# Kernel optimization log

Measured on AMD Instinct MI355X. Metric: run time of the kernel, lower is better.

The kernel has to match this reference:

```python
import jax, jax.numpy as jnp
import numpy as np

V, H, L = 32000, 2048, 4
B, S = 4, 1024


def setup_inputs() -> dict:
    key = jax.random.key(0)
    ks = jax.random.split(key, 10)
    input_ids = jax.random.randint(ks[0], (B, S), 0, V)
    emb = jax.random.normal(ks[1], (V, H), dtype=jnp.float32)
    # ternary quantized weights in {-1, 0, +1}, stored as int8
    layer_wq = jax.random.randint(ks[2], (L, H, H), -1, 2).astype(jnp.int8)
    layer_scale = jax.random.normal(ks[3], (L, H, 1), dtype=jnp.float32)
    layer_bias = jax.random.normal(ks[4], (L, H), dtype=jnp.float32)
    out_wq = jax.random.randint(ks[5], (V, H), -1, 2).astype(jnp.int8)
    out_scale = jax.random.normal(ks[6], (V, 1), dtype=jnp.float32)
    out_bias = jax.random.normal(ks[7], (V,), dtype=jnp.float32)
    return {
        "input_ids": input_ids,
        "emb": emb,
        "layer_wq": layer_wq,
        "layer_scale": layer_scale,
        "layer_bias": layer_bias,
        "out_wq": out_wq,
        "out_scale": out_scale,
        "out_bias": out_bias,
    }


def _bit_linear(x, wq, scale, bias):
    # dequantize ternary int8 weight: [out,in] * [out,1] -> fp32, then x @ W^T + b
    w = wq.astype(jnp.float32) * scale
    return jnp.einsum("bsh,oh->bso", x, w) + bias


def reference(input_ids, emb, layer_wq, layer_scale, layer_bias, out_wq, out_scale, out_bias):
    x = emb[input_ids]  # [B,S,H]
    for i in range(L):
        x = jax.nn.relu(_bit_linear(x, layer_wq[i], layer_scale[i], layer_bias[i]))
    logits = _bit_linear(x, out_wq, out_scale, out_bias)  # [B,S,V]
    return logits
```

## Files before the change

kernel.cpp:

```cpp
#include <hip/hip_runtime.h>
#include <hip/hip_bf16.h>
#include <stdint.h>
#include <stddef.h>

#define GLOBAL_AS __attribute__((address_space(1)))
#define LDS_AS __attribute__((address_space(3)))

typedef __attribute__((ext_vector_type(4))) float f32x4;
typedef __attribute__((ext_vector_type(8))) short bf16x8;
typedef __attribute__((ext_vector_type(4))) int   i32x4;

template<int N> struct ICn { static constexpr int value = N; };

__device__ __forceinline__ unsigned short f2bf(float f) {
  unsigned u = __float_as_uint(f);
  u += 0x7FFFu + ((u >> 16) & 1u);
  return (unsigned short)(u >> 16);
}

__device__ __forceinline__ void load_lds16(const void* g, void* l) {
  __builtin_amdgcn_global_load_lds((const GLOBAL_AS void*)g, (LDS_AS void*)l, 16, 0, 0);
}

template<int IMM, typename T>
__device__ __forceinline__ void ds_read128t(T &d, unsigned addr) {
  asm volatile("ds_read_b128 %0, %1 offset:%c2"
               : "=&v"(d) : "v"(addr), "i"(IMM));
}

__global__ __launch_bounds__(256) void detect_dtype_k(const int* __restrict__ w,
                                                      int* __restrict__ flag) {
  __shared__ int bad;
  if (threadIdx.x == 0) bad = 0;
  __syncthreads();
  int b = 0;
  for (int i = threadIdx.x; i < 4096; i += 256) {
    int v = w[i];
    if (v < -1 || v > 1) b = 1;
  }
  if (b) bad = 1;
  __syncthreads();
  if (threadIdx.x == 0) *flag = bad ? 0 : 1;
}

__global__ __launch_bounds__(256) void gather_emb_k(const int* __restrict__ ids,
                                                    const float* __restrict__ emb,
                                                    unsigned short* __restrict__ x) {
  const int t = blockIdx.x;
  const int row = ids[t];
  const float4* src = (const float4*)(emb + (size_t)row * 2048);
  const int e = threadIdx.x;
  float4 a = src[e * 2], b = src[e * 2 + 1];
  uint4 o;
  o.x = f2bf(a.x) | ((unsigned)f2bf(a.y) << 16);
  o.y = f2bf(a.z) | ((unsigned)f2bf(a.w) << 16);
  o.z = f2bf(b.x) | ((unsigned)f2bf(b.y) << 16);
  o.w = f2bf(b.z) | ((unsigned)f2bf(b.w) << 16);
  *(uint4*)(x + (size_t)t * 2048 + e * 8) = o;
}

__global__ __launch_bounds__(256) void convert_w_k(const void* __restrict__ src,
                                                   unsigned short* __restrict__ dst,
                                                   const int* __restrict__ flag) {
  const long long idx = ((long long)blockIdx.x * 256 + threadIdx.x) * 8;
  int v[8];
  if (*flag) {
    const int* s = (const int*)src + idx;
    const int4 a = *(const int4*)s;
    const int4 b = *(const int4*)(s + 4);
    v[0] = a.x; v[1] = a.y; v[2] = a.z; v[3] = a.w;
    v[4] = b.x; v[5] = b.y; v[6] = b.z; v[7] = b.w;
  } else {
    const uint2 u = *(const uint2*)((const char*)src + idx);
    v[0] = (char)(u.x); v[1] = (char)(u.x >> 8); v[2] = (char)(u.x >> 16); v[3] = (char)(u.x >> 24);
    v[4] = (char)(u.y); v[5] = (char)(u.y >> 8); v[6] = (char)(u.y >> 16); v[7] = (char)(u.y >> 24);
  }
  unsigned short o[8];
  #pragma unroll
  for (int k = 0; k < 8; ++k)
    o[k] = (v[k] == 0) ? 0 : ((v[k] > 0) ? 0x3F80 : 0xBF80);
  uint4 w;
  w.x = o[0] | ((unsigned)o[1] << 16);
  w.y = o[2] | ((unsigned)o[3] << 16);
  w.z = o[4] | ((unsigned)o[5] << 16);
  w.w = o[6] | ((unsigned)o[7] << 16);
  *(uint4*)(dst + idx) = w;
}

__global__ __launch_bounds__(256) void pack_w8_k(const void* __restrict__ src,
                                                 signed char* __restrict__ dst,
                                                 const int* __restrict__ flag) {
  const long long idx = ((long long)blockIdx.x * 256 + threadIdx.x) * 8;
  if (*flag) {
    const int* s = (const int*)src + idx;
    const int4 a = *(const int4*)s;
    const int4 b = *(const int4*)(s + 4);
    uint2 o;
    o.x = ((unsigned)(unsigned char)(signed char)a.x)       |
          ((unsigned)(unsigned char)(signed char)a.y << 8)  |
          ((unsigned)(unsigned char)(signed char)a.z << 16) |
          ((unsigned)(unsigned char)(signed char)a.w << 24);
    o.y = ((unsigned)(unsigned char)(signed char)b.x)       |
          ((unsigned)(unsigned char)(signed char)b.y << 8)  |
          ((unsigned)(unsigned char)(signed char)b.z << 16) |
          ((unsigned)(unsigned char)(signed char)b.w << 24);
    *(uint2*)(dst + idx) = o;
  } else {
    *(uint2*)(dst + idx) = *(const uint2*)((const char*)src + idx);
  }
}

__global__ __launch_bounds__(256) void colsum_k(const signed char* __restrict__ w,
                                                float* __restrict__ cs) {
  const int lane = threadIdx.x & 63;
  const int c = blockIdx.x * 4 + (threadIdx.x >> 6);
  const int4* p = (const int4*)(w + (size_t)c * 2048 + lane * 32);
  const int4 a = p[0], b = p[1];
  int wds[8] = {a.x, a.y, a.z, a.w, b.x, b.y, b.z, b.w};
  int s = 0;
  #pragma unroll
  for (int k = 0; k < 8; ++k)
    #pragma unroll
    for (int bb = 0; bb < 4; ++bb)
      s += (signed char)(wds[k] >> (8 * bb));
  #pragma unroll
  for (int o = 32; o; o >>= 1) s += __shfl_xor(s, o);
  if (lane == 0) cs[c] = (float)s;
}

__global__ __launch_bounds__(256) void rowquant_k(const unsigned short* __restrict__ x,
                                                  signed char* __restrict__ xq,
                                                  float* __restrict__ srow) {
  __shared__ float wmax[4];
  const int r = blockIdx.x;
  const int e = threadIdx.x;
  const uint4 u = *(const uint4*)(x + (size_t)r * 2048 + e * 8);
  unsigned wds[4] = {u.x, u.y, u.z, u.w};
  float v[8];
  #pragma unroll
  for (int k = 0; k < 4; ++k) {
    v[2 * k]     = __uint_as_float(wds[k] << 16);
    v[2 * k + 1] = __uint_as_float(wds[k] & 0xFFFF0000u);
  }
  float m = 0.0f;
  #pragma unroll
  for (int k = 0; k < 8; ++k) m = fmaxf(m, v[k]);
  #pragma unroll
  for (int o = 32; o; o >>= 1) m = fmaxf(m, __shfl_xor(m, o));
  if ((threadIdx.x & 63) == 0) wmax[threadIdx.x >> 6] = m;
  __syncthreads();
  const float mx = fmaxf(fmaxf(wmax[0], wmax[1]), fmaxf(wmax[2], wmax[3]));
  const float inv = mx > 0.0f ? 255.0f / mx : 0.0f;
  unsigned b[8];
  #pragma unroll
  for (int k = 0; k < 8; ++k) {
    int q = __float2int_rn(v[k] * inv - 127.5f);
    q = q < -128 ? -128 : (q > 127 ? 127 : q);
    b[k] = (unsigned)(unsigned char)(signed char)q;
  }
  uint2 o;
  o.x = b[0] | (b[1] << 8) | (b[2] << 16) | (b[3] << 24);
  o.y = b[4] | (b[5] << 8) | (b[6] << 16) | (b[7] << 24);
  *(uint2*)(xq + (size_t)r * 2048 + e * 8) = o;
  if (threadIdx.x == 0) srow[r] = mx * (1.0f / 255.0f);
}

__global__ __launch_bounds__(256) void gemm_bt_k(
    const unsigned short* __restrict__ A,
    const unsigned short* __restrict__ Bw,
    const float* __restrict__ scale,
    const float* __restrict__ bias,
    unsigned short* __restrict__ Cout,
    int M, int N, int K)
{
  __shared__ unsigned short As[128 * 64];
  __shared__ unsigned short Bs[128 * 64];

  const int tid  = threadIdx.x;
  const int lane = tid & 63;
  const int wid  = tid >> 6;
  const int wm   = wid >> 1;
  const int wn   = wid & 1;

  const int mBase = blockIdx.y * 128;
  const int nBase = blockIdx.x * 128;

  const int srow = lane >> 3;
  const int skel = (lane & 7) * 8;

  f32x4 acc[4][4];
  #pragma unroll
  for (int i = 0; i < 4; ++i)
    #pragma unroll
    for (int j = 0; j < 4; ++j)
      acc[i][j] = (f32x4){0.f, 0.f, 0.f, 0.f};

  for (int k0 = 0; k0 < K; k0 += 64) {
    #pragma unroll
    for (int j = 0; j < 4; ++j) {
      const int c = wid * 4 + j;
      const int row = c * 8 + srow;
      load_lds16(A  + (size_t)(mBase + row) * K + (k0 + skel), As + c * 512);
      load_lds16(Bw + (size_t)(nBase + row) * K + (k0 + skel), Bs + c * 512);
    }
    __syncthreads();

    #pragma unroll
    for (int s = 0; s < 2; ++s) {
      const int kk = s * 32 + (lane >> 4) * 8;
      bf16x8 af[4], bfr[4];
      #pragma unroll
      for (int i = 0; i < 4; ++i)
        af[i] = *(const bf16x8*)(As + (wm * 64 + i * 16 + (lane & 15)) * 64 + kk);
      #pragma unroll
      for (int j = 0; j < 4; ++j)
        bfr[j] = *(const bf16x8*)(Bs + (wn * 64 + j * 16 + (lane & 15)) * 64 + kk);
      #pragma unroll
      for (int i = 0; i < 4; ++i)
        #pragma unroll
        for (int j = 0; j < 4; ++j)
          acc[i][j] = __builtin_amdgcn_mfma_f32_16x16x32_bf16(af[i], bfr[j], acc[i][j], 0, 0, 0);
    }
    __syncthreads();
  }

  const int lr = lane >> 4;
  const int lc = lane & 15;
  #pragma unroll
  for (int j = 0; j < 4; ++j) {
    const int col = nBase + wn * 64 + j * 16 + lc;
    const float sc = scale[col];
    const float bs = bias[col];
    #pragma unroll
    for (int i = 0; i < 4; ++i) {
      const int r0 = mBase + wm * 64 + i * 16 + lr * 4;
      #pragma unroll
      for (int r = 0; r < 4; ++r) {
        float vv = fmaxf(acc[i][j][r] * sc + bs, 0.0f);
        Cout[(size_t)(r0 + r) * N + col] = f2bf(vv);
      }
    }
  }
}


#define RD_B8() do { \
  ds_read128t<PAR*32768 +    0>(bfr[0][0], vB0); ds_read128t<PAR*32768 +    0>(bfr[0][1], vB1); \
  ds_read128t<PAR*32768 + 2048>(bfr[1][0], vB0); ds_read128t<PAR*32768 + 2048>(bfr[1][1], vB1); \
  ds_read128t<PAR*32768 + 4096>(bfr[2][0], vB0); ds_read128t<PAR*32768 + 4096>(bfr[2][1], vB1); \
  ds_read128t<PAR*32768 + 6144>(bfr[3][0], vB0); ds_read128t<PAR*32768 + 6144>(bfr[3][1], vB1); \
} while (0)

#define RD_A2(dst, R) do { \
  ds_read128t<PAR*32768 + (R)*2048       >(dst[0][0], vA0); ds_read128t<PAR*32768 + (R)*2048       >(dst[0][1], vA1); \
  ds_read128t<PAR*32768 + (R)*2048 + 2048>(dst[1][0], vA0); ds_read128t<PAR*32768 + (R)*2048 + 2048>(dst[1][1], vA1); \
} while (0)

#define STAGE_A(h) do { if (t >= 1 && t + 1 < nt) { \
  load_lds16(pA[h][0], As + (PAR ^ 1) * 32768 + (h) * 16384 +        wid * 1024); \
  load_lds16(pA[h][1], As + (PAR ^ 1) * 32768 + (h) * 16384 + 8192 + wid * 1024); \
  pA[h][0] += 128; pA[h][1] += 128; } } while (0)

#define STAGE_B(h) do { if (t + 2 < nt) { \
  load_lds16(pB[h][0], Bs + PAR * 32768 + (h) * 16384 +        wid * 1024); \
  load_lds16(pB[h][1], Bs + PAR * 32768 + (h) * 16384 + 8192 + wid * 1024); \
  pB[h][0] += 128; pB[h][1] += 128; } } while (0)

#define SBAR0 __builtin_amdgcn_sched_barrier(0)

#define LGKM_WAIT(LG) \
  SBAR0; \
  asm volatile("s_waitcnt lgkmcnt(" #LG ")" ::: "memory"); \
  SBAR0;

#define MFMA_PH(IP, AF) \
  __builtin_amdgcn_s_setprio(1); \
  { _Pragma("unroll") for (int ii = 0; ii < 2; ++ii) { \
      _Pragma("unroll") for (int j = 0; j < 4; ++j) { \
        acc[(IP)*2+ii][j] = __builtin_amdgcn_mfma_i32_16x16x64_i8(AF[ii][0], bfr[j][0], acc[(IP)*2+ii][j], 0, 0, 0); \
        acc[(IP)*2+ii][j] = __builtin_amdgcn_mfma_i32_16x16x64_i8(AF[ii][1], bfr[j][1], acc[(IP)*2+ii][j], 0, 0, 0); \
  } } } \
  __builtin_amdgcn_s_setprio(0); \
  SBAR0;

__global__ __launch_bounds__(512) void gemm256i8_k(
    const signed char* __restrict__ Aq,
    const signed char* __restrict__ Bq,
    const float* __restrict__ scale,
    const float* __restrict__ bias,
    const float* __restrict__ srow,
    const float* __restrict__ colsum,
    float* __restrict__ C,
    int M, int N, int K)
{
  __shared__ signed char As[2 * 32768];
  __shared__ signed char Bs[2 * 32768];

  const int tid  = threadIdx.x;
  const int lane = tid & 63;
  const int wid  = tid >> 6;
  const int wm   = wid >> 2;
  const int wn   = wid & 3;
  const int l15  = lane & 15;
  const int l4   = lane >> 4;

  const int q    = gridDim.x >> 3;
  const int wgid = (blockIdx.x & 7) * q + (blockIdx.x >> 3);
  const int mBase = (wgid & 15) << 8;
  const int nBase = (wgid >> 4) << 8;

  const int gsw = ((lane & 7) ^ (lane >> 3)) * 16;

  const unsigned asB = (unsigned)(size_t)(const LDS_AS signed char*)As;
  const unsigned bsB = (unsigned)(size_t)(const LDS_AS signed char*)Bs;
  const unsigned x7  = (unsigned)(l15 & 7);
  const unsigned vA0 = asB + (wm << 14) + l15 * 128 + ((((unsigned)l4    ) ^ x7) << 4);
  const unsigned vA1 = asB + (wm << 14) + l15 * 128 + ((((unsigned)l4 + 4) ^ x7) << 4);
  const unsigned vB0 = bsB + (wn << 13) + l15 * 128 + ((((unsigned)l4    ) ^ x7) << 4);
  const unsigned vB1 = bsB + (wn << 13) + l15 * 128 + ((((unsigned)l4 + 4) ^ x7) << 4);

  const signed char* pA[2][2];
  const signed char* pB[2][2];
  #pragma unroll
  for (int h = 0; h < 2; ++h)
    #pragma unroll
    for (int j = 0; j < 2; ++j) {
      const int row = h * 128 + j * 64 + wid * 8 + (lane >> 3);
      pA[h][j] = Aq + (size_t)(mBase + row) * K + gsw;
      pB[h][j] = Bq + (size_t)(nBase + row) * K + gsw;
    }

  i32x4 acc[8][4];
  #pragma unroll
  for (int i = 0; i < 8; ++i)
    #pragma unroll
    for (int j = 0; j < 4; ++j)
      acc[i][j] = (i32x4){0, 0, 0, 0};

  const int nt = K >> 7;

  #pragma unroll
  for (int h = 0; h < 2; ++h)
    #pragma unroll
    for (int j = 0; j < 2; ++j)
      load_lds16(pA[h][j], As + h * 16384 + j * 8192 + wid * 1024);
  #pragma unroll
  for (int h = 0; h < 2; ++h)
    #pragma unroll
    for (int j = 0; j < 2; ++j)
      load_lds16(pB[h][j], Bs + h * 16384 + j * 8192 + wid * 1024);
  #pragma unroll
  for (int h = 0; h < 2; ++h)
    #pragma unroll
    for (int j = 0; j < 2; ++j)
      load_lds16(pA[h][j] + 128, As + 32768 + h * 16384 + j * 8192 + wid * 1024);
  #pragma unroll
  for (int h = 0; h < 2; ++h)
    #pragma unroll
    for (int j = 0; j < 2; ++j)
      load_lds16(pB[h][j] + 128, Bs + 32768 + h * 16384 + j * 8192 + wid * 1024);
  #pragma unroll
  for (int h = 0; h < 2; ++h)
    #pragma unroll
    for (int j = 0; j < 2; ++j) { pA[h][j] += 256; pB[h][j] += 256; }

  asm volatile("s_waitcnt vmcnt(8)" ::: "memory");
  __builtin_amdgcn_s_barrier();

  i32x4 bfr[4][2];
  i32x4 afP[2][2], afQ[2][2];

  auto tile_body = [&](int t, auto par_c) {
    constexpr int PAR = decltype(par_c)::value;
    RD_A2(afP, 0);
    RD_B8();
    RD_A2(afQ, 2);
    STAGE_A(0);
    LGKM_WAIT(4)
    MFMA_PH(0, afP)
    RD_A2(afP, 4);
    STAGE_A(1);
    LGKM_WAIT(4)
    MFMA_PH(1, afQ)
    __builtin_amdgcn_s_barrier();
    RD_A2(afQ, 6);
    STAGE_B(0);
    LGKM_WAIT(4)
    MFMA_PH(2, afP)
    STAGE_B(1);
    LGKM_WAIT(0)
    MFMA_PH(3, afQ)
    if (t + 2 < nt) asm volatile("s_waitcnt vmcnt(4)" ::: "memory");
    else            asm volatile("s_waitcnt vmcnt(0)" ::: "memory");
    __builtin_amdgcn_s_barrier();
  };

  for (int t = 0; t < nt; t += 2) {
    tile_body(t,     ICn<0>{});
    tile_body(t + 1, ICn<1>{});
  }

  #pragma unroll
  for (int j = 0; j < 4; ++j) {
    const int col = nBase + wn * 64 + j * 16 + l15;
    const float sc  = scale[col];
    const float csc = colsum[col] * sc;
    const float bs  = bias[col];
    #pragma unroll
    for (int i = 0; i < 8; ++i) {
      const int r0 = mBase + wm * 128 + i * 16 + l4 * 4;
      const f32x4 sv = *(const f32x4*)(srow + r0);
      #pragma unroll
      for (int r = 0; r < 4; ++r) {
        const float fa = (float)acc[i][j][r];
        C[(size_t)(r0 + r) * N + col] =
            fmaf(fa, sv[r] * sc, fmaf(127.5f * sv[r], csc, bs));
      }
    }
  }
}

extern "C" void kernel_launch(void* const* d_in, const int* in_sizes, int n_in,
                              void* d_out, int out_size, void* d_ws, size_t ws_size,
                              hipStream_t stream) {
  const int V = 32000, H = 2048, L = 4, M = 4096;
  const int*   ids         = (const int*)d_in[0];
  const float* emb         = (const float*)d_in[1];
  const void*  layer_wq    = d_in[2];
  const float* layer_scale = (const float*)d_in[3];
  const float* layer_bias  = (const float*)d_in[4];
  const void*  out_wq      = d_in[5];
  const float* out_scale   = (const float*)d_in[6];
  const float* out_bias    = (const float*)d_in[7];
  float* out = (float*)d_out;

  char* ws = (char*)d_ws;
  const size_t xBytes = (size_t)M * H * 2;
  unsigned short* xA  = (unsigned short*)(ws);
  unsigned short* xB  = (unsigned short*)(ws + xBytes);
  unsigned short* lw  = (unsigned short*)(ws + 2 * xBytes);
  size_t off = 2 * xBytes + (size_t)L * H * H * 2;
  signed char* ow8    = (signed char*)(ws + off);   off += (size_t)V * H;
  signed char* xq     = (signed char*)(ws + off);   off += (size_t)M * H;
  float* srow         = (float*)(ws + off);         off += (size_t)M * 4;
  float* cs           = (float*)(ws + off);         off += (size_t)V * 4;
  int* flag           = (int*)(ws + off);

  detect_dtype_k<<<1, 256, 0, stream>>>((const int*)layer_wq, flag);
  gather_emb_k<<<M, 256, 0, stream>>>(ids, emb, xA);
  convert_w_k<<<(L * H * H) / 2048, 256, 0, stream>>>(layer_wq, lw, flag);
  pack_w8_k<<<(V * H) / 2048, 256, 0, stream>>>(out_wq, ow8, flag);
  colsum_k<<<V / 4, 256, 0, stream>>>(ow8, cs);

  dim3 blk(256);
  dim3 gh(H / 128, M / 128);
  unsigned short* xin = xA;
  unsigned short* xout = xB;
  for (int i = 0; i < L; ++i) {
    gemm_bt_k<<<gh, blk, 0, stream>>>(xin, lw + (size_t)i * H * H,
                                      layer_scale + i * H, layer_bias + i * H,
                                      xout, M, H, H);
    unsigned short* t = xin; xin = xout; xout = t;
  }

  rowquant_k<<<M, 256, 0, stream>>>(xin, xq, srow);

  gemm256i8_k<<<dim3(2000), dim3(512), 0, stream>>>(
      xq, ow8, out_scale, out_bias, srow, cs, out, M, V, H);
}
```

Baseline: 715.6 us.

## Load A fragments directly from global, triple-buffer B in LDS, skip int8 repack copy

The int8 output GEMM stops staging activation tiles in LDS. Each wave now loads its A fragments straight from global memory into registers with global_load_dwordx4, while B tiles use a three-stage LDS ring. Launch bounds now ask for two workgroups per CU. The pack kernel returns early when the weights are already int8, and colsum and the GEMM read the raw weights directly, avoiding a 65MB copy. The risks are uncoalesced global loads for A, more vector registers, and vmcnt accounting that now mixes A register loads with B LDS loads.

After: 990.2 us. 1.38x slower.

```diff
diff --git a/kernel.cpp b/kernel.cpp
--- a/kernel.cpp
+++ b/kernel.cpp
@@ -10,8 +10,6 @@
 typedef __attribute__((ext_vector_type(8))) short bf16x8;
 typedef __attribute__((ext_vector_type(4))) int   i32x4;
 
-template<int N> struct ICn { static constexpr int value = N; };
-
 __device__ __forceinline__ unsigned short f2bf(float f) {
   unsigned u = __float_as_uint(f);
   u += 0x7FFFu + ((u >> 16) & 1u);
@@ -25,6 +23,12 @@
 template<int IMM, typename T>
 __device__ __forceinline__ void ds_read128t(T &d, unsigned addr) {
   asm volatile("ds_read_b128 %0, %1 offset:%c2"
+               : "=&v"(d) : "v"(addr), "i"(IMM));
+}
+
+template<int IMM>
+__device__ __forceinline__ void gload16(i32x4 &d, unsigned long long addr) {
+  asm volatile("global_load_dwordx4 %0, %1, off offset:%c2"
                : "=&v"(d) : "v"(addr), "i"(IMM));
 }
 
@@ -90,28 +94,28 @@
 __global__ __launch_bounds__(256) void pack_w8_k(const void* __restrict__ src,
                                                  signed char* __restrict__ dst,
                                                  const int* __restrict__ flag) {
+  if (!*flag) return;
   const long long idx = ((long long)blockIdx.x * 256 + threadIdx.x) * 8;
-  if (*flag) {
-    const int* s = (const int*)src + idx;
-    const int4 a = *(const int4*)s;
-    const int4 b = *(const int4*)(s + 4);
-    uint2 o;
-    o.x = ((unsigned)(unsigned char)(signed char)a.x)       |
-          ((unsigned)(unsigned char)(signed char)a.y << 8)  |
-          ((unsigned)(unsigned char)(signed char)a.z << 16) |
-          ((unsigned)(unsigned char)(signed char)a.w << 24);
-    o.y = ((unsigned)(unsigned char)(signed char)b.x)       |
-          ((unsigned)(unsigned char)(signed char)b.y << 8)  |
-          ((unsigned)(unsigned char)(signed char)b.z << 16) |
-          ((unsigned)(unsigned char)(signed char)b.w << 24);
-    *(uint2*)(dst + idx) = o;
-  } else {
-    *(uint2*)(dst + idx) = *(const uint2*)((const char*)src + idx);
-  }
-}
-
-__global__ __launch_bounds__(256) void colsum_k(const signed char* __restrict__ w,
+  const int* s = (const int*)src + idx;
+  const int4 a = *(const int4*)s;
+  const int4 b = *(const int4*)(s + 4);
+  uint2 o;
+  o.x = ((unsigned)(unsigned char)(signed char)a.x)       |
+        ((unsigned)(unsigned char)(signed char)a.y << 8)  |
+        ((unsigned)(unsigned char)(signed char)a.z << 16) |
+        ((unsigned)(unsigned char)(signed char)a.w << 24);
+  o.y = ((unsigned)(unsigned char)(signed char)b.x)       |
+        ((unsigned)(unsigned char)(signed char)b.y << 8)  |
+        ((unsigned)(unsigned char)(signed char)b.z << 16) |
+        ((unsigned)(unsigned char)(signed char)b.w << 24);
+  *(uint2*)(dst + idx) = o;
+}
+
+__global__ __launch_bounds__(256) void colsum_k(const signed char* __restrict__ wp,
+                                                const signed char* __restrict__ wr,
+                                                const int* __restrict__ flag,
                                                 float* __restrict__ cs) {
+  const signed char* w = (*flag) ? wp : wr;
   const int lane = threadIdx.x & 63;
   const int c = blockIdx.x * 4 + (threadIdx.x >> 6);
   const int4* p = (const int4*)(w + (size_t)c * 2048 + lane * 32);
@@ -244,36 +248,27 @@
 }
 
 
-#define RD_B8() do { \
-  ds_read128t<PAR*32768 +    0>(bfr[0][0], vB0); ds_read128t<PAR*32768 +    0>(bfr[0][1], vB1); \
-  ds_read128t<PAR*32768 + 2048>(bfr[1][0], vB0); ds_read128t<PAR*32768 + 2048>(bfr[1][1], vB1); \
-  ds_read128t<PAR*32768 + 4096>(bfr[2][0], vB0); ds_read128t<PAR*32768 + 4096>(bfr[2][1], vB1); \
-  ds_read128t<PAR*32768 + 6144>(bfr[3][0], vB0); ds_read128t<PAR*32768 + 6144>(bfr[3][1], vB1); \
+#define SBAR0 __builtin_amdgcn_sched_barrier(0)
+
+#define DS8(A0, A1) do { \
+  ds_read128t<0   >(bfr[0][0], A0); ds_read128t<0   >(bfr[0][1], A1); \
+  ds_read128t<2048>(bfr[1][0], A0); ds_read128t<2048>(bfr[1][1], A1); \
+  ds_read128t<4096>(bfr[2][0], A0); ds_read128t<4096>(bfr[2][1], A1); \
+  ds_read128t<6144>(bfr[3][0], A0); ds_read128t<6144>(bfr[3][1], A1); \
 } while (0)
 
-#define RD_A2(dst, R) do { \
-  ds_read128t<PAR*32768 + (R)*2048       >(dst[0][0], vA0); ds_read128t<PAR*32768 + (R)*2048       >(dst[0][1], vA1); \
-  ds_read128t<PAR*32768 + (R)*2048 + 2048>(dst[1][0], vA0); ds_read128t<PAR*32768 + (R)*2048 + 2048>(dst[1][1], vA1); \
+#define AL4(DST, I0, I1) do { \
+  gload16<0 >(DST[0][0], aaddr[I0]); gload16<64>(DST[0][1], aaddr[I0]); \
+  gload16<0 >(DST[1][0], aaddr[I1]); gload16<64>(DST[1][1], aaddr[I1]); \
 } while (0)
 
-#define STAGE_A(h) do { if (t >= 1 && t + 1 < nt) { \
-  load_lds16(pA[h][0], As + (PAR ^ 1) * 32768 + (h) * 16384 +        wid * 1024); \
-  load_lds16(pA[h][1], As + (PAR ^ 1) * 32768 + (h) * 16384 + 8192 + wid * 1024); \
-  pA[h][0] += 128; pA[h][1] += 128; } } while (0)
-
-#define STAGE_B(h) do { if (t + 2 < nt) { \
-  load_lds16(pB[h][0], Bs + PAR * 32768 + (h) * 16384 +        wid * 1024); \
-  load_lds16(pB[h][1], Bs + PAR * 32768 + (h) * 16384 + 8192 + wid * 1024); \
-  pB[h][0] += 128; pB[h][1] += 128; } } while (0)
-
-#define SBAR0 __builtin_amdgcn_sched_barrier(0)
-
-#define LGKM_WAIT(LG) \
-  SBAR0; \
-  asm volatile("s_waitcnt lgkmcnt(" #LG ")" ::: "memory"); \
-  SBAR0;
-
-#define MFMA_PH(IP, AF) \
+#define WAITV(N) do { SBAR0; \
+  asm volatile("s_waitcnt vmcnt(" #N ")" ::: "memory"); SBAR0; } while (0)
+
+#define WAITVL(N) do { SBAR0; \
+  asm volatile("s_waitcnt vmcnt(" #N ") lgkmcnt(0)" ::: "memory"); SBAR0; } while (0)
+
+#define MFMA_PH(IP, AF) do { \
   __builtin_amdgcn_s_setprio(1); \
   { _Pragma("unroll") for (int ii = 0; ii < 2; ++ii) { \
       _Pragma("unroll") for (int j = 0; j < 4; ++j) { \
@@ -281,11 +276,22 @@
         acc[(IP)*2+ii][j] = __builtin_amdgcn_mfma_i32_16x16x64_i8(AF[ii][1], bfr[j][1], acc[(IP)*2+ii][j], 0, 0, 0); \
   } } } \
   __builtin_amdgcn_s_setprio(0); \
-  SBAR0;
-
-__global__ __launch_bounds__(512) void gemm256i8_k(
+  SBAR0; \
+} while (0)
+
+#define STAGE_B4(DSTBYTES, GUARDSRC) do { \
+  load_lds16(GUARDSRC(0), (DSTBYTES) +         wid * 1024); \
+  load_lds16(GUARDSRC(1), (DSTBYTES) +  8192 + wid * 1024); \
+  load_lds16(GUARDSRC(2), (DSTBYTES) + 16384 + wid * 1024); \
+  load_lds16(GUARDSRC(3), (DSTBYTES) + 24576 + wid * 1024); \
+  pB[0] += 128; pB[1] += 128; pB[2] += 128; pB[3] += 128; \
+} while (0)
+
+__global__ __launch_bounds__(512, 2) void gemm256i8_k(
     const signed char* __restrict__ Aq,
-    const signed char* __restrict__ Bq,
+    const signed char* __restrict__ Bpk,
+    const signed char* __restrict__ Braw,
+    const int* __restrict__ flag,
     const float* __restrict__ scale,
     const float* __restrict__ bias,
     const float* __restrict__ srow,
@@ -293,8 +299,9 @@
     float* __restrict__ C,
     int M, int N, int K)
 {
-  __shared__ signed char As[2 * 32768];
-  __shared__ signed char Bs[2 * 32768];
+  __shared__ signed char Bs[3 * 32768];
+
+  const signed char* Bq = (*flag) ? Bpk : Braw;
 
   const int tid  = threadIdx.x;
   const int lane = tid & 63;
@@ -311,24 +318,22 @@
 
   const int gsw = ((lane & 7) ^ (lane >> 3)) * 16;
 
-  const unsigned asB = (unsigned)(size_t)(const LDS_AS signed char*)As;
   const unsigned bsB = (unsigned)(size_t)(const LDS_AS signed char*)Bs;
   const unsigned x7  = (unsigned)(l15 & 7);
-  const unsigned vA0 = asB + (wm << 14) + l15 * 128 + ((((unsigned)l4    ) ^ x7) << 4);
-  const unsigned vA1 = asB + (wm << 14) + l15 * 128 + ((((unsigned)l4 + 4) ^ x7) << 4);
   const unsigned vB0 = bsB + (wn << 13) + l15 * 128 + ((((unsigned)l4    ) ^ x7) << 4);
   const unsigned vB1 = bsB + (wn << 13) + l15 * 128 + ((((unsigned)l4 + 4) ^ x7) << 4);
 
-  const signed char* pA[2][2];
-  const signed char* pB[2][2];
-  #pragma unroll
-  for (int h = 0; h < 2; ++h)
-    #pragma unroll
-    for (int j = 0; j < 2; ++j) {
-      const int row = h * 128 + j * 64 + wid * 8 + (lane >> 3);
-      pA[h][j] = Aq + (size_t)(mBase + row) * K + gsw;
-      pB[h][j] = Bq + (size_t)(nBase + row) * K + gsw;
-    }
+  const signed char* pB[4];
+  #pragma unroll
+  for (int j = 0; j < 4; ++j)
+    pB[j] = Bq + (size_t)(nBase + j * 64 + wid * 8 + (lane >> 3)) * K + gsw;
+
+  unsigned long long aaddr[8];
+  #pragma unroll
+  for (int i = 0; i < 8; ++i) {
+    aaddr[i] = (unsigned long long)(size_t)(Aq + (size_t)(mBase + wm * 128 + i * 16 + l15) * K + l4 * 16);
+    if (i >= 2) aaddr[i] -= 128;
+  }
 
   i32x4 acc[8][4];
   #pragma unroll
@@ -339,66 +344,49 @@
 
   const int nt = K >> 7;
 
-  #pragma unroll
-  for (int h = 0; h < 2; ++h)
-    #pragma unroll
-    for (int j = 0; j < 2; ++j)
-      load_lds16(pA[h][j], As + h * 16384 + j * 8192 + wid * 1024);
-  #pragma unroll
-  for (int h = 0; h < 2; ++h)
-    #pragma unroll
-    for (int j = 0; j < 2; ++j)
-      load_lds16(pB[h][j], Bs + h * 16384 + j * 8192 + wid * 1024);
-  #pragma unroll
-  for (int h = 0; h < 2; ++h)
-    #pragma unroll
-    for (int j = 0; j < 2; ++j)
-      load_lds16(pA[h][j] + 128, As + 32768 + h * 16384 + j * 8192 + wid * 1024);
-  #pragma unroll
-  for (int h = 0; h < 2; ++h)
-    #pragma unroll
-    for (int j = 0; j < 2; ++j)
-      load_lds16(pB[h][j] + 128, Bs + 32768 + h * 16384 + j * 8192 + wid * 1024);
-  #pragma unroll
-  for (int h = 0; h < 2; ++h)
-    #pragma unroll
-    for (int j = 0; j < 2; ++j) { pA[h][j] += 256; pB[h][j] += 256; }
-
-  asm volatile("s_waitcnt vmcnt(8)" ::: "memory");
-  __builtin_amdgcn_s_barrier();
-
   i32x4 bfr[4][2];
   i32x4 afP[2][2], afQ[2][2];
 
-  auto tile_body = [&](int t, auto par_c) {
-    constexpr int PAR = decltype(par_c)::value;
-    RD_A2(afP, 0);
-    RD_B8();
-    RD_A2(afQ, 2);
-    STAGE_A(0);
-    LGKM_WAIT(4)
-    MFMA_PH(0, afP)
-    RD_A2(afP, 4);
-    STAGE_A(1);
-    LGKM_WAIT(4)
-    MFMA_PH(1, afQ)
+#define SRC_PLAIN(J) pB[J]
+  STAGE_B4((signed char*)Bs, SRC_PLAIN);
+  SBAR0;
+  STAGE_B4((signed char*)Bs + 32768, SRC_PLAIN);
+  SBAR0;
+  AL4(afP, 0, 1);
+  WAITV(8);
+  __builtin_amdgcn_s_barrier();
+
+  for (int t = 0; t < nt; ++t) {
+    const unsigned sOff = (unsigned)(t % 3) * 32768u;
+    signed char* bDst = (signed char*)Bs + (size_t)(((t + 2) % 3)) * 32768;
+    const bool stOK = (t + 2 < nt);
+#define SRC_GUARD(J) (stOK ? pB[J] : Bq)
+
+    #pragma unroll
+    for (int i = 2; i < 8; ++i) aaddr[i] += 128;
+    const unsigned a0 = vB0 + sOff;
+    const unsigned a1 = vB1 + sOff;
+
+    DS8(a0, a1);
+    AL4(afQ, 2, 3);
+    SBAR0;
+    STAGE_B4(bDst, SRC_GUARD);
+    WAITVL(8);
+    MFMA_PH(0, afP);
+    AL4(afP, 4, 5);
+    WAITV(8);
+    MFMA_PH(1, afQ);
+    AL4(afQ, 6, 7);
+    WAITV(4);
+    MFMA_PH(2, afP);
+    aaddr[0] += 128; aaddr[1] += 128;
+    AL4(afP, 0, 1);
+    WAITV(4);
+    MFMA_PH(3, afQ);
     __builtin_amdgcn_s_barrier();
-    RD_A2(afQ, 6);
-    STAGE_B(0);
-    LGKM_WAIT(4)
-    MFMA_PH(2, afP)
-    STAGE_B(1);
-    LGKM_WAIT(0)
-    MFMA_PH(3, afQ)
-    if (t + 2 < nt) asm volatile("s_waitcnt vmcnt(4)" ::: "memory");
-    else            asm volatile("s_waitcnt vmcnt(0)" ::: "memory");
-    __builtin_amdgcn_s_barrier();
-  };
-
-  for (int t = 0; t < nt; t += 2) {
-    tile_body(t,     ICn<0>{});
-    tile_body(t + 1, ICn<1>{});
-  }
+  }
+
+  WAITVL(0);
 
   #pragma unroll
   for (int j = 0; j < 4; ++j) {
@@ -450,7 +438,7 @@
   gather_emb_k<<<M, 256, 0, stream>>>(ids, emb, xA);
   convert_w_k<<<(L * H * H) / 2048, 256, 0, stream>>>(layer_wq, lw, flag);
   pack_w8_k<<<(V * H) / 2048, 256, 0, stream>>>(out_wq, ow8, flag);
-  colsum_k<<<V / 4, 256, 0, stream>>>(ow8, cs);
+  colsum_k<<<V / 4, 256, 0, stream>>>(ow8, (const signed char*)out_wq, flag, cs);
 
   dim3 blk(256);
   dim3 gh(H / 128, M / 128);
@@ -466,5 +454,6 @@
   rowquant_k<<<M, 256, 0, stream>>>(xin, xq, srow);
 
   gemm256i8_k<<<dim3(2000), dim3(512), 0, stream>>>(
-      xq, ow8, out_scale, out_bias, srow, cs, out, M, V, H);
-}
+      xq, ow8, (const signed char*)out_wq, flag,
+      out_scale, out_bias, srow, cs, out, M, V, H);
+}
```

## Double-buffer and swizzle the bf16 hidden-layer GEMM; skip the int8 weight copy

Applied to the files above, without the earlier changes.

Rewrites the hidden-layer bf16 GEMM to double-buffer its LDS tiles with direct global-to-LDS loads, so the next K-tile is fetched while MFMAs run on the current one. It also adds an XOR swizzle to reduce LDS bank conflicts, explicit waitcnt and priority scheduling, and an occupancy hint of 2 blocks per CU. When the output weights are already int8, the pack kernel now returns early and colsum and the int8 GEMM read the raw weights directly, removing a full copy. The change adds LDS use and complexity, and the dummy loads issued on the last iteration waste a little bandwidth.

After: 631.1 us (median of 3 runs). -11.8%, faster.

```diff
diff --git a/kernel.cpp b/kernel.cpp
--- a/kernel.cpp
+++ b/kernel.cpp
@@ -27,6 +27,17 @@
   asm volatile("ds_read_b128 %0, %1 offset:%c2"
                : "=&v"(d) : "v"(addr), "i"(IMM));
 }
+
+#define SBAR0 __builtin_amdgcn_sched_barrier(0)
+
+#define WAITV(N) do { SBAR0; \
+  asm volatile("s_waitcnt vmcnt(" #N ")" ::: "memory"); SBAR0; } while (0)
+
+#define WAITVL(N) do { SBAR0; \
+  asm volatile("s_waitcnt vmcnt(" #N ") lgkmcnt(0)" ::: "memory"); SBAR0; } while (0)
+
+#define LGKMW(N) do { SBAR0; \
+  asm volatile("s_waitcnt lgkmcnt(" #N ")" ::: "memory"); SBAR0; } while (0)
 
 __global__ __launch_bounds__(256) void detect_dtype_k(const int* __restrict__ w,
                                                       int* __restrict__ flag) {
@@ -90,28 +101,28 @@
 __global__ __launch_bounds__(256) void pack_w8_k(const void* __restrict__ src,
                                                  signed char* __restrict__ dst,
                                                  const int* __restrict__ flag) {
+  if (!*flag) return;
   const long long idx = ((long long)blockIdx.x * 256 + threadIdx.x) * 8;
-  if (*flag) {
-    const int* s = (const int*)src + idx;
-    const int4 a = *(const int4*)s;
-    const int4 b = *(const int4*)(s + 4);
-    uint2 o;
-    o.x = ((unsigned)(unsigned char)(signed char)a.x)       |
-          ((unsigned)(unsigned char)(signed char)a.y << 8)  |
-          ((unsigned)(unsigned char)(signed char)a.z << 16) |
-          ((unsigned)(unsigned char)(signed char)a.w << 24);
-    o.y = ((unsigned)(unsigned char)(signed char)b.x)       |
-          ((unsigned)(unsigned char)(signed char)b.y << 8)  |
-          ((unsigned)(unsigned char)(signed char)b.z << 16) |
-          ((unsigned)(unsigned char)(signed char)b.w << 24);
-    *(uint2*)(dst + idx) = o;
-  } else {
-    *(uint2*)(dst + idx) = *(const uint2*)((const char*)src + idx);
-  }
-}
-
-__global__ __launch_bounds__(256) void colsum_k(const signed char* __restrict__ w,
+  const int* s = (const int*)src + idx;
+  const int4 a = *(const int4*)s;
+  const int4 b = *(const int4*)(s + 4);
+  uint2 o;
+  o.x = ((unsigned)(unsigned char)(signed char)a.x)       |
+        ((unsigned)(unsigned char)(signed char)a.y << 8)  |
+        ((unsigned)(unsigned char)(signed char)a.z << 16) |
+        ((unsigned)(unsigned char)(signed char)a.w << 24);
+  o.y = ((unsigned)(unsigned char)(signed char)b.x)       |
+        ((unsigned)(unsigned char)(signed char)b.y << 8)  |
+        ((unsigned)(unsigned char)(signed char)b.z << 16) |
+        ((unsigned)(unsigned char)(signed char)b.w << 24);
+  *(uint2*)(dst + idx) = o;
+}
+
+__global__ __launch_bounds__(256) void colsum_k(const signed char* __restrict__ wp,
+                                                const signed char* __restrict__ wr,
+                                                const int* __restrict__ flag,
                                                 float* __restrict__ cs) {
+  const signed char* w = (*flag) ? wp : wr;
   const int lane = threadIdx.x & 63;
   const int c = blockIdx.x * 4 + (threadIdx.x >> 6);
   const int4* p = (const int4*)(w + (size_t)c * 2048 + lane * 32);
@@ -165,7 +176,7 @@
   if (threadIdx.x == 0) srow[r] = mx * (1.0f / 255.0f);
 }
 
-__global__ __launch_bounds__(256) void gemm_bt_k(
+__global__ __launch_bounds__(256, 2) void gemm_bt2_k(
     const unsigned short* __restrict__ A,
     const unsigned short* __restrict__ Bw,
     const float* __restrict__ scale,
@@ -173,20 +184,38 @@
     unsigned short* __restrict__ Cout,
     int M, int N, int K)
 {
-  __shared__ unsigned short As[128 * 64];
-  __shared__ unsigned short Bs[128 * 64];
+  __shared__ unsigned short As[2 * 8192];
+  __shared__ unsigned short Bs[2 * 8192];
 
   const int tid  = threadIdx.x;
   const int lane = tid & 63;
   const int wid  = tid >> 6;
   const int wm   = wid >> 1;
   const int wn   = wid & 1;
+  const int l15  = lane & 15;
+  const int l4   = lane >> 4;
 
   const int mBase = blockIdx.y * 128;
   const int nBase = blockIdx.x * 128;
 
-  const int srow = lane >> 3;
-  const int skel = (lane & 7) * 8;
+  const int gsw = ((lane & 7) ^ (lane >> 3)) * 8;
+
+  const unsigned asB = (unsigned)(size_t)(const LDS_AS unsigned short*)As;
+  const unsigned bsB = (unsigned)(size_t)(const LDS_AS unsigned short*)Bs;
+  const unsigned x7  = (unsigned)(l15 & 7);
+  const unsigned vA0 = asB + (wm << 13) + l15 * 128 + ((((unsigned)l4    ) ^ x7) << 4);
+  const unsigned vA1 = asB + (wm << 13) + l15 * 128 + ((((unsigned)l4 + 4) ^ x7) << 4);
+  const unsigned vB0 = bsB + (wn << 13) + l15 * 128 + ((((unsigned)l4    ) ^ x7) << 4);
+  const unsigned vB1 = bsB + (wn << 13) + l15 * 128 + ((((unsigned)l4 + 4) ^ x7) << 4);
+
+  const unsigned short* pA[4];
+  const unsigned short* pB[4];
+  #pragma unroll
+  for (int j = 0; j < 4; ++j) {
+    const int row = (wid * 4 + j) * 8 + (lane >> 3);
+    pA[j] = A  + (size_t)(mBase + row) * K + gsw;
+    pB[j] = Bw + (size_t)(nBase + row) * K + gsw;
+  }
 
   f32x4 acc[4][4];
   #pragma unroll
@@ -195,37 +224,70 @@
     for (int j = 0; j < 4; ++j)
       acc[i][j] = (f32x4){0.f, 0.f, 0.f, 0.f};
 
-  for (int k0 = 0; k0 < K; k0 += 64) {
-    #pragma unroll
-    for (int j = 0; j < 4; ++j) {
-      const int c = wid * 4 + j;
-      const int row = c * 8 + srow;
-      load_lds16(A  + (size_t)(mBase + row) * K + (k0 + skel), As + c * 512);
-      load_lds16(Bw + (size_t)(nBase + row) * K + (k0 + skel), Bs + c * 512);
-    }
-    __syncthreads();
-
-    #pragma unroll
-    for (int s = 0; s < 2; ++s) {
-      const int kk = s * 32 + (lane >> 4) * 8;
-      bf16x8 af[4], bfr[4];
-      #pragma unroll
-      for (int i = 0; i < 4; ++i)
-        af[i] = *(const bf16x8*)(As + (wm * 64 + i * 16 + (lane & 15)) * 64 + kk);
+  const int nt = K >> 6;
+
+  #pragma unroll
+  for (int j = 0; j < 4; ++j)
+    load_lds16(pA[j], As + (wid * 4 + j) * 512);
+  #pragma unroll
+  for (int j = 0; j < 4; ++j)
+    load_lds16(pB[j], Bs + (wid * 4 + j) * 512);
+  #pragma unroll
+  for (int j = 0; j < 4; ++j) { pA[j] += 64; pB[j] += 64; }
+  WAITV(0);
+  __builtin_amdgcn_s_barrier();
+
+  bf16x8 afA[4], afB[4], bfrA[4], bfrB[4];
+
+  for (int t = 0; t < nt; ++t) {
+    const unsigned po = (unsigned)(t & 1) * 16384u;
+    const unsigned aA0 = vA0 + po, aA1 = vA1 + po;
+    const unsigned aB0 = vB0 + po, aB1 = vB1 + po;
+    unsigned short* dA = As + (size_t)((t + 1) & 1) * 8192;
+    unsigned short* dB = Bs + (size_t)((t + 1) & 1) * 8192;
+    const bool st = (t + 1 < nt);
+
+    ds_read128t<0   >(afA[0], aA0); ds_read128t<2048>(afA[1], aA0);
+    ds_read128t<4096>(afA[2], aA0); ds_read128t<6144>(afA[3], aA0);
+    ds_read128t<0   >(bfrA[0], aB0); ds_read128t<2048>(bfrA[1], aB0);
+    ds_read128t<4096>(bfrA[2], aB0); ds_read128t<6144>(bfrA[3], aB0);
+    ds_read128t<0   >(afB[0], aA1); ds_read128t<2048>(afB[1], aA1);
+    ds_read128t<4096>(afB[2], aA1); ds_read128t<6144>(afB[3], aA1);
+    ds_read128t<0   >(bfrB[0], aB1); ds_read128t<2048>(bfrB[1], aB1);
+    ds_read128t<4096>(bfrB[2], aB1); ds_read128t<6144>(bfrB[3], aB1);
+    #pragma unroll
+    for (int j = 0; j < 4; ++j)
+      load_lds16(st ? pA[j] : A, dA + (wid * 4 + j) * 512);
+    #pragma unroll
+    for (int j = 0; j < 4; ++j)
+      load_lds16(st ? pB[j] : Bw, dB + (wid * 4 + j) * 512);
+    #pragma unroll
+    for (int j = 0; j < 4; ++j) { pA[j] += 64; pB[j] += 64; }
+
+    LGKMW(8);
+    __builtin_amdgcn_s_setprio(1);
+    #pragma unroll
+    for (int i = 0; i < 4; ++i)
       #pragma unroll
       for (int j = 0; j < 4; ++j)
-        bfr[j] = *(const bf16x8*)(Bs + (wn * 64 + j * 16 + (lane & 15)) * 64 + kk);
+        acc[i][j] = __builtin_amdgcn_mfma_f32_16x16x32_bf16(afA[i], bfrA[j], acc[i][j], 0, 0, 0);
+    __builtin_amdgcn_s_setprio(0);
+    SBAR0;
+    LGKMW(0);
+    __builtin_amdgcn_s_setprio(1);
+    #pragma unroll
+    for (int i = 0; i < 4; ++i)
       #pragma unroll
-      for (int i = 0; i < 4; ++i)
-        #pragma unroll
-        for (int j = 0; j < 4; ++j)
-          acc[i][j] = __builtin_amdgcn_mfma_f32_16x16x32_bf16(af[i], bfr[j], acc[i][j], 0, 0, 0);
-    }
-    __syncthreads();
-  }
-
-  const int lr = lane >> 4;
-  const int lc = lane & 15;
+      for (int j = 0; j < 4; ++j)
+        acc[i][j] = __builtin_amdgcn_mfma_f32_16x16x32_bf16(afB[i], bfrB[j], acc[i][j], 0, 0, 0);
+    __builtin_amdgcn_s_setprio(0);
+    SBAR0;
+    WAITV(0);
+    __builtin_amdgcn_s_barrier();
+  }
+
+  const int lr = l4;
+  const int lc = l15;
   #pragma unroll
   for (int j = 0; j < 4; ++j) {
     const int col = nBase + wn * 64 + j * 16 + lc;
@@ -257,23 +319,16 @@
 } while (0)
 
 #define STAGE_A(h) do { if (t >= 1 && t + 1 < nt) { \
-  load_lds16(pA[h][0], As + (PAR ^ 1) * 32768 + (h) * 16384 +        wid * 1024); \
-  load_lds16(pA[h][1], As + (PAR ^ 1) * 32768 + (h) * 16384 + 8192 + wid * 1024); \
+  load_lds16(pA[h][0], Asf + (PAR ^ 1) * 32768 + (h) * 16384 +        wid * 1024); \
+  load_lds16(pA[h][1], Asf + (PAR ^ 1) * 32768 + (h) * 16384 + 8192 + wid * 1024); \
   pA[h][0] += 128; pA[h][1] += 128; } } while (0)
 
 #define STAGE_B(h) do { if (t + 2 < nt) { \
-  load_lds16(pB[h][0], Bs + PAR * 32768 + (h) * 16384 +        wid * 1024); \
-  load_lds16(pB[h][1], Bs + PAR * 32768 + (h) * 16384 + 8192 + wid * 1024); \
+  load_lds16(pB[h][0], Bsf + PAR * 32768 + (h) * 16384 +        wid * 1024); \
+  load_lds16(pB[h][1], Bsf + PAR * 32768 + (h) * 16384 + 8192 + wid * 1024); \
   pB[h][0] += 128; pB[h][1] += 128; } } while (0)
 
-#define SBAR0 __builtin_amdgcn_sched_barrier(0)
-
-#define LGKM_WAIT(LG) \
-  SBAR0; \
-  asm volatile("s_waitcnt lgkmcnt(" #LG ")" ::: "memory"); \
-  SBAR0;
-
-#define MFMA_PH(IP, AF) \
+#define MFMA_PH(IP, AF) do { \
   __builtin_amdgcn_s_setprio(1); \
   { _Pragma("unroll") for (int ii = 0; ii < 2; ++ii) { \
       _Pragma("unroll") for (int j = 0; j < 4; ++j) { \
@@ -281,11 +336,14 @@
         acc[(IP)*2+ii][j] = __builtin_amdgcn_mfma_i32_16x16x64_i8(AF[ii][1], bfr[j][1], acc[(IP)*2+ii][j], 0, 0, 0); \
   } } } \
   __builtin_amdgcn_s_setprio(0); \
-  SBAR0;
-
-__global__ __launch_bounds__(512) void gemm256i8_k(
+  SBAR0; \
+} while (0)
+
+__global__ __launch_bounds__(512, 2) void gemm256i8_k(
     const signed char* __restrict__ Aq,
-    const signed char* __restrict__ Bq,
+    const signed char* __restrict__ Bpk,
+    const signed char* __restrict__ Braw,
+    const int* __restrict__ flag,
     const float* __restrict__ scale,
     const float* __restrict__ bias,
     const float* __restrict__ srow,
@@ -293,8 +351,10 @@
     float* __restrict__ C,
     int M, int N, int K)
 {
-  __shared__ signed char As[2 * 32768];
-  __shared__ signed char Bs[2 * 32768];
+  __shared__ signed char Asf[2 * 32768];
+  __shared__ signed char Bsf[2 * 32768];
+
+  const signed char* Bq = (*flag) ? Bpk : Braw;
 
   const int tid  = threadIdx.x;
   const int lane = tid & 63;
@@ -311,8 +371,8 @@
 
   const int gsw = ((lane & 7) ^ (lane >> 3)) * 16;
 
-  const unsigned asB = (unsigned)(size_t)(const LDS_AS signed char*)As;
-  const unsigned bsB = (unsigned)(size_t)(const LDS_AS signed char*)Bs;
+  const unsigned asB = (unsigned)(size_t)(const LDS_AS signed char*)Asf;
+  const unsigned bsB = (unsigned)(size_t)(const LDS_AS signed char*)Bsf;
   const unsigned x7  = (unsigned)(l15 & 7);
   const unsigned vA0 = asB + (wm << 14) + l15 * 128 + ((((unsigned)l4    ) ^ x7) << 4);
   const unsigned vA1 = asB + (wm << 14) + l15 * 128 + ((((unsigned)l4 + 4) ^ x7) << 4);
@@ -343,22 +403,22 @@
   for (int h = 0; h < 2; ++h)
     #pragma unroll
     for (int j = 0; j < 2; ++j)
-      load_lds16(pA[h][j], As + h * 16384 + j * 8192 + wid * 1024);
+      load_lds16(pA[h][j], Asf + h * 16384 + j * 8192 + wid * 1024);
   #pragma unroll
   for (int h = 0; h < 2; ++h)
     #pragma unroll
     for (int j = 0; j < 2; ++j)
-      load_lds16(pB[h][j], Bs + h * 16384 + j * 8192 + wid * 1024);
+      load_lds16(pB[h][j], Bsf + h * 16384 + j * 8192 + wid * 1024);
   #pragma unroll
   for (int h = 0; h < 2; ++h)
     #pragma unroll
     for (int j = 0; j < 2; ++j)
-      load_lds16(pA[h][j] + 128, As + 32768 + h * 16384 + j * 8192 + wid * 1024);
+      load_lds16(pA[h][j] + 128, Asf + 32768 + h * 16384 + j * 8192 + wid * 1024);
   #pragma unroll
   for (int h = 0; h < 2; ++h)
     #pragma unroll
     for (int j = 0; j < 2; ++j)
-      load_lds16(pB[h][j] + 128, Bs + 32768 + h * 16384 + j * 8192 + wid * 1024);
+      load_lds16(pB[h][j] + 128, Bsf + 32768 + h * 16384 + j * 8192 + wid * 1024);
   #pragma unroll
   for (int h = 0; h < 2; ++h)
     #pragma unroll
@@ -376,22 +436,22 @@
     RD_B8();
     RD_A2(afQ, 2);
     STAGE_A(0);
-    LGKM_WAIT(4)
-    MFMA_PH(0, afP)
+    LGKMW(4);
+    MFMA_PH(0, afP);
     RD_A2(afP, 4);
     STAGE_A(1);
-    LGKM_WAIT(4)
-    MFMA_PH(1, afQ)
+    LGKMW(4);
+    MFMA_PH(1, afQ);
     __builtin_amdgcn_s_barrier();
     RD_A2(afQ, 6);
     STAGE_B(0);
-    LGKM_WAIT(4)
-    MFMA_PH(2, afP)
+    LGKMW(4);
+    MFMA_PH(2, afP);
     STAGE_B(1);
-    LGKM_WAIT(0)
-    MFMA_PH(3, afQ)
-    if (t + 2 < nt) asm volatile("s_waitcnt vmcnt(4)" ::: "memory");
-    else            asm volatile("s_waitcnt vmcnt(0)" ::: "memory");
+    LGKMW(0);
+    MFMA_PH(3, afQ);
+    if (t + 2 < nt) { WAITV(4); }
+    else            { WAITV(0); }
     __builtin_amdgcn_s_barrier();
   };
 
@@ -450,21 +510,22 @@
   gather_emb_k<<<M, 256, 0, stream>>>(ids, emb, xA);
   convert_w_k<<<(L * H * H) / 2048, 256, 0, stream>>>(layer_wq, lw, flag);
   pack_w8_k<<<(V * H) / 2048, 256, 0, stream>>>(out_wq, ow8, flag);
-  colsum_k<<<V / 4, 256, 0, stream>>>(ow8, cs);
+  colsum_k<<<V / 4, 256, 0, stream>>>(ow8, (const signed char*)out_wq, flag, cs);
 
   dim3 blk(256);
   dim3 gh(H / 128, M / 128);
   unsigned short* xin = xA;
   unsigned short* xout = xB;
   for (int i = 0; i < L; ++i) {
-    gemm_bt_k<<<gh, blk, 0, stream>>>(xin, lw + (size_t)i * H * H,
-                                      layer_scale + i * H, layer_bias + i * H,
-                                      xout, M, H, H);
+    gemm_bt2_k<<<gh, blk, 0, stream>>>(xin, lw + (size_t)i * H * H,
+                                       layer_scale + i * H, layer_bias + i * H,
+                                       xout, M, H, H);
     unsigned short* t = xin; xin = xout; xout = t;
   }
 
   rowquant_k<<<M, 256, 0, stream>>>(xin, xq, srow);
 
   gemm256i8_k<<<dim3(2000), dim3(512), 0, stream>>>(
-      xq, ow8, out_scale, out_bias, srow, cs, out, M, V, H);
-}
+      xq, ow8, (const signed char*)out_wq, flag,
+      out_scale, out_bias, srow, cs, out, M, V, H);
+}
```
